# Kernel optimization log

Hardware: AMD Instinct MI355X
Metric: run time of the kernel (lower is better)

Reference implementation:

```python
import jax, jax.numpy as jnp
import numpy as np

B, N, CS, CZ, H, CH, G, P = 2, 384, 384, 128, 8, 16, 2, 8
CZ4 = CZ // 4
INF = 1e5
UMAX = 3.0     # self.u_max
LMAX = 2.0     # self.log_scale_max
SQRT_CH = CH ** 0.5


def quat_to_rot(q):
    q = q / jnp.linalg.norm(q, axis=-1, keepdims=True)
    w, x, y, z = q[..., 0], q[..., 1], q[..., 2], q[..., 3]
    R = jnp.stack([
        1 - 2 * (y * y + z * z), 2 * (x * y - w * z), 2 * (x * z + w * y),
        2 * (x * y + w * z), 1 - 2 * (x * x + z * z), 2 * (y * z - w * x),
        2 * (x * z - w * y), 2 * (y * z + w * x), 1 - 2 * (x * x + y * y)], axis=-1)
    return R.reshape(q.shape[:-1] + (3, 3))


def robust_nll(delta, sigma):
    # inline robust 3x3 Cholesky solve: dist_sq = d^T S^-1 d, log_det = ln|S|
    eps = 1e-8
    s00 = sigma[..., 0, 0]; s01 = sigma[..., 0, 1]; s02 = sigma[..., 0, 2]
    s11 = sigma[..., 1, 1]; s12 = sigma[..., 1, 2]; s22 = sigma[..., 2, 2]
    d0 = delta[..., 0]; d1 = delta[..., 1]; d2 = delta[..., 2]
    l00_sq = jnp.maximum(s00, eps); inv_l00 = jax.lax.rsqrt(l00_sq)
    l10 = s01 * inv_l00; l20 = s02 * inv_l00
    l11_sq = jnp.maximum(s11 - l10 * l10, eps); inv_l11 = jax.lax.rsqrt(l11_sq)
    l21 = (s12 - l20 * l10) * inv_l11
    l22_sq = jnp.maximum(s22 - l20 * l20 - l21 * l21, eps); inv_l22 = jax.lax.rsqrt(l22_sq)
    log_det = jnp.log(l00_sq) + jnp.log(l11_sq) + jnp.log(l22_sq)
    y0 = d0 * inv_l00
    y1 = (d1 - l10 * y0) * inv_l11
    y2 = (d2 - l20 * y0 - l21 * y1) * inv_l22
    return y0 * y0 + y1 * y1 + y2 * y2, log_det


def iga_forward(s, z, mask, rot, trans, local_mean, scaling_log,
                Wq, Wk, Wv, Wb, bb, Wdz, bdz, Wqg, bqg, Wkg, bkg,
                Wvp, bvp, geo_scale, geo_bias, Wout, bout):
    # scalar q/k/v: [B,H,N,CH]
    q = (s @ Wq).reshape(B, N, H, CH).transpose(0, 2, 1, 3)
    k = (s @ Wk).reshape(B, N, H, CH).transpose(0, 2, 1, 3)
    v = (s @ Wv).reshape(B, N, H, CH).transpose(0, 2, 1, 3)
    logits = jnp.einsum('bhid,bhjd->bhij', q, k) / SQRT_CH
    # pair bias: [B,H,N,N]
    logits = logits + (z @ Wb + bb).transpose(0, 3, 1, 2)

    def parse(feat):  # -> u [B,N,H,G,3], s_log_delta [B,N,H,G,3]
        raw = feat.reshape(B, N, H, G, 6)
        return jnp.tanh(raw[..., :3]) * UMAX, jnp.tanh(raw[..., 3:]) * LMAX

    def to_global(u, sld):
        anchor = local_mean[:, :, None, None, :]
        base = scaling_log[:, :, None, None, :]
        sig_loc = jnp.maximum(jnp.exp(base + sld), 1e-6)
        pos = anchor + u * sig_loc
        mu = jnp.einsum('bnij,bnhgj->bnhgi', rot, pos) + trans[:, :, None, None, :]
        var = jnp.exp(2.0 * (base + sld))
        Sig = jnp.einsum('bnij,bnhgj,bnkj->bnhgik', rot, var, rot)  # R diag(var) R^T
        return mu.transpose(0, 2, 1, 3, 4), Sig.transpose(0, 2, 1, 3, 4, 5)

    qu, qs = parse(s @ Wqg + bqg)
    ku, ks = parse(s @ Wkg + bkg)
    q_mu, q_sig = to_global(qu, qs)   # [B,H,N,G,3], [B,H,N,G,3,3]
    k_mu, k_sig = to_global(ku, ks)
    delta = q_mu[:, :, :, None] - k_mu[:, :, None, :]      # [B,H,N,N,G,3]
    ssum = q_sig[:, :, :, None] + k_sig[:, :, None, :]     # [B,H,N,N,G,3,3]
    dist_sq, log_det = robust_nll(delta, ssum)
    geo = (-0.5 * dist_sq - 0.5 * log_det).sum(-1)          # [B,H,N,N]

    mask2d = mask[:, None, :, None] * mask[:, None, None, :]  # [B,1,N,N]
    a = jax.nn.softplus(geo_scale)[None, :, None, None]
    G_geo = a * (geo * mask2d) + geo_bias[None, :, None, None]
    logits = logits + G_geo + (1.0 - mask2d) * (-INF)
    w = jax.nn.softmax(logits, axis=-1)                      # [B,H,N,N]

    # scalar output
    o = jnp.einsum('bhij,bhjd->bihd', w, v).reshape(B, N, H * CH)
    # point output (IPA-style): to global, attend, back to local frame
    vpts = (s @ Wvp + bvp).reshape(B, N, H, P, 3)
    vpg = jnp.einsum('bnij,bnhpj->bnhpi', rot, vpts) + trans[:, :, None, None, :]
    vpg = vpg.transpose(0, 2, 1, 3, 4)                       # [B,H,N,P,3]
    opt = jnp.einsum('bhij,bhjpc->bhipc', w, vpg)            # [B,H,N,P,3]
    opt_local = jnp.einsum('bnji,bhnpj->bnhpi', rot, opt - trans[:, None, :, None, :])
    onorm = jnp.sqrt((opt_local ** 2).sum(-1) + 1e-8)        # [B,N,H,P]
    # pair output
    pz = z @ Wdz + bdz                                       # [B,N,N,CZ4]
    opair = jnp.einsum('bhij,bijc->bihc', w, pz)             # [B,N,H,CZ4]

    cat = jnp.concatenate([o, opt_local.reshape(B, N, H * P * 3),
                           onorm.reshape(B, N, H * P),
                           opair.reshape(B, N, H * CZ4)], axis=-1)  # [B,N,640]
    return cat @ Wout + bout


def setup_inputs() -> dict:
    ks = jax.random.split(jax.random.key(0), 24)
    rnd = lambda i, shape, sc=1.0: jax.random.normal(ks[i], shape, dtype=jnp.float32) * sc
    w = 0.02
    return dict(
        s=rnd(0, (B, N, CS)), z=rnd(1, (B, N, N, CZ)),
        mask=jnp.ones((B, N), jnp.float32),
        rot=quat_to_rot(rnd(2, (B, N, 4))),
        trans=rnd(3, (B, N, 3), 1.0),
        local_mean=rnd(4, (B, N, 3), 0.5),
        scaling_log=rnd(5, (B, N, 3), 0.1),
        Wq=rnd(6, (CS, H * CH), w), Wk=rnd(7, (CS, H * CH), w), Wv=rnd(8, (CS, H * CH), w),
        Wb=rnd(9, (CZ, H), w), bb=rnd(10, (H,), w),
        Wdz=rnd(11, (CZ, CZ4), w), bdz=rnd(12, (CZ4,), w),
        Wqg=rnd(13, (CS, H * G * 6), w), bqg=rnd(14, (H * G * 6,), w),
        Wkg=rnd(15, (CS, H * G * 6), w), bkg=rnd(16, (H * G * 6,), w),
        Wvp=rnd(17, (CS, H * P * 3), w), bvp=rnd(18, (H * P * 3,), w),
        geo_scale=jnp.ones((H,), jnp.float32), geo_bias=jnp.zeros((H,), jnp.float32),
        Wout=rnd(19, (H * (CH + P * 4 + CZ4), CS), w), bout=jnp.zeros((CS,), jnp.float32))


def reference(s, z, mask, rot, trans, local_mean, scaling_log, Wq, Wk, Wv, Wb, bb,
              Wdz, bdz, Wqg, bqg, Wkg, bkg, Wvp, bvp, geo_scale, geo_bias, Wout, bout):
    return iga_forward(s, z, mask, rot, trans, local_mean, scaling_log, Wq, Wk, Wv,
                       Wb, bb, Wdz, bdz, Wqg, bqg, Wkg, bkg, Wvp, bvp,
                       geo_scale, geo_bias, Wout, bout)
```

## Files before the change

kernel.cpp:

```cpp
#include <hip/hip_runtime.h>
#include <hip/hip_fp16.h>

#define NB   2
#define NN   384
#define NCS  384
#define NCZ  128
#define NH   8
#define NCH  16
#define NG   2
#define NP   8
#define NCZ4 32
#define BN   (NB*NN)
#define LINW 768
#define PZROW ((size_t)BN*NN)

typedef _Float16 f16x8 __attribute__((ext_vector_type(8)));
typedef float    f32x4 __attribute__((ext_vector_type(4)));

__global__ void k_wprep(const float* __restrict__ Wb, const float* __restrict__ Wdz,
                        _Float16* __restrict__ wf) {
    int t = threadIdx.x;
    for (int e = t; e < 12*64*8; e += 256) {
        int r = e & 7, lane = (e >> 3) & 63, nk = e >> 9;
        int n = nk >> 2, kk = nk & 3;
        int c = kk*32 + (lane >> 4)*8 + r;
        int col = n*16 + (lane & 15);
        float w;
        if      (col < 8)  w = Wb[c*NH + col];
        else if (col < 40) w = Wdz[c*NCZ4 + (col-8)];
        else               w = 0.f;
        wf[e] = (_Float16)w;
    }
}

__global__ void __launch_bounds__(256, 2)
k_zproj(const float* __restrict__ z, const _Float16* __restrict__ wf,
        const float* __restrict__ bb, const float* __restrict__ bdz,
        float* __restrict__ zbg, __half* __restrict__ pzg2) {
    __shared__ __align__(16) _Float16 zh[64*128];
    __shared__ float  zbT[8][64];
    __shared__ __half pzt[64][34];
    __shared__ float  bias_s[48];

    int t = threadIdx.x;
    int lane = t & 63, w = t >> 6;
    int bi = blockIdx.x / 6, ch = blockIdx.x % 6;
    const float* zbase = z + ((size_t)bi*NN + ch*64)*NCZ;

    const float* src = zbase + (size_t)(t >> 5)*NCZ + (t & 31)*4;
    float4 pre[8];
    #pragma unroll
    for (int p = 0; p < 8; ++p) pre[p] = *(const float4*)(src + (size_t)(p*8)*NCZ);

    f16x8 bfr[12];
    #pragma unroll
    for (int nk = 0; nk < 12; ++nk)
        bfr[nk] = ((const f16x8*)wf)[nk*64 + lane];
    if (t < 48) bias_s[t] = (t < 8) ? bb[t] : ((t < 40) ? bdz[t-8] : 0.f);

    int srow0 = t >> 5;
    int scb   = (t & 31) * 8;
    int sswz  = (srow0 & 7) << 4;
    #pragma unroll
    for (int p = 0; p < 8; ++p) {
        union { _Float16 h[4]; unsigned long long u; } pk;
        pk.h[0] = (_Float16)pre[p].x; pk.h[1] = (_Float16)pre[p].y;
        pk.h[2] = (_Float16)pre[p].z; pk.h[3] = (_Float16)pre[p].w;
        *(unsigned long long*)((char*)zh + (p*8 + srow0)*256 + (scb ^ sswz)) = pk.u;
    }
    __syncthreads();

    int arow  = w*16 + (lane & 15);
    int abase = arow*256 + ((lane >> 4) << 4);
    int akey  = (lane & 7) << 4;
    int ccol  = lane & 15;
    int cjl   = w*16 + (lane >> 4)*4;
    f16x8 af0 = *(const f16x8*)((const char*)zh + ((abase +   0) ^ akey));
    f16x8 af1 = *(const f16x8*)((const char*)zh + ((abase +  64) ^ akey));
    f16x8 af2 = *(const f16x8*)((const char*)zh + ((abase + 128) ^ akey));
    f16x8 af3 = *(const f16x8*)((const char*)zh + ((abase + 192) ^ akey));
    f32x4 ac0 = {0.f,0.f,0.f,0.f}, ac1 = ac0, ac2 = ac0;
    ac0 = __builtin_amdgcn_mfma_f32_16x16x32_f16(af0, bfr[0], ac0, 0,0,0);
    ac1 = __builtin_amdgcn_mfma_f32_16x16x32_f16(af0, bfr[4], ac1, 0,0,0);
    ac2 = __builtin_amdgcn_mfma_f32_16x16x32_f16(af0, bfr[8], ac2, 0,0,0);
    ac0 = __builtin_amdgcn_mfma_f32_16x16x32_f16(af1, bfr[1], ac0, 0,0,0);
    ac1 = __builtin_amdgcn_mfma_f32_16x16x32_f16(af1, bfr[5], ac1, 0,0,0);
    ac2 = __builtin_amdgcn_mfma_f32_16x16x32_f16(af1, bfr[9], ac2, 0,0,0);
    ac0 = __builtin_amdgcn_mfma_f32_16x16x32_f16(af2, bfr[2], ac0, 0,0,0);
    ac1 = __builtin_amdgcn_mfma_f32_16x16x32_f16(af2, bfr[6], ac1, 0,0,0);
    ac2 = __builtin_amdgcn_mfma_f32_16x16x32_f16(af2, bfr[10], ac2, 0,0,0);
    ac0 = __builtin_amdgcn_mfma_f32_16x16x32_f16(af3, bfr[3], ac0, 0,0,0);
    ac1 = __builtin_amdgcn_mfma_f32_16x16x32_f16(af3, bfr[7], ac1, 0,0,0);
    ac2 = __builtin_amdgcn_mfma_f32_16x16x32_f16(af3, bfr[11], ac2, 0,0,0);
    #pragma unroll
    for (int r = 0; r < 4; ++r) {
        int j = cjl + r;
        float v0 = ac0[r] + bias_s[ccol];
        if (ccol < 8) zbT[ccol][j] = v0;
        else          pzt[j][ccol-8] = __float2half(v0);
        pzt[j][ccol+8] = __float2half(ac1[r] + bias_s[16+ccol]);
        if (ccol < 8)
            pzt[j][ccol+24] = __float2half(ac2[r] + bias_s[32+ccol]);
    }
    __syncthreads();

    {
        int e = t*2, h = e >> 6, j = e & 63;
        float2 v; v.x = zbT[h][j]; v.y = zbT[h][j+1];
        *(float2*)(zbg + ((size_t)bi*NH + h)*NN + ch*64 + j) = v;
    }
    {
        int cp = t >> 4, l = t & 15, j0 = l*4;
        union { __half2 h2[4]; float4 f4; } u;
        #pragma unroll
        for (int r = 0; r < 4; ++r) {
            int j = j0 + r;
            u.h2[r] = __halves2half2(pzt[j][2*cp], pzt[j][2*cp+1]);
        }
        __half2* dst = (__half2*)pzg2 + (size_t)cp*PZROW + (size_t)bi*NN + ch*64 + j0;
        *(float4*)dst = u.f4;
    }
}

__global__ void k_rowlin(const float* __restrict__ s,
                         const float* __restrict__ Wq, const float* __restrict__ Wk,
                         const float* __restrict__ Wv,
                         const float* __restrict__ Wqg, const float* __restrict__ bqg,
                         const float* __restrict__ Wkg, const float* __restrict__ bkg,
                         const float* __restrict__ Wvp, const float* __restrict__ bvp,
                         float* __restrict__ lin,
                         float* __restrict__ kT, float* __restrict__ vT) {
    __shared__ float sl[4][NCS];
    int t  = threadIdx.x;
    int r0 = blockIdx.x * 4;
    for (int idx = t; idx < 4*NCS; idx += 256)
        sl[idx / NCS][idx % NCS] = s[(size_t)(r0 + idx/NCS)*NCS + (idx % NCS)];
    __syncthreads();
    int col = blockIdx.y * 256 + t;
    const float* W; int sw; float bias = 0.f;
    if      (col < 128) { W = Wq  + col;        sw = 128; }
    else if (col < 256) { W = Wk  + (col-128);  sw = 128; }
    else if (col < 384) { W = Wv  + (col-256);  sw = 128; }
    else if (col < 480) { W = Wqg + (col-384);  sw = 96;  bias = bqg[col-384]; }
    else if (col < 576) { W = Wkg + (col-480);  sw = 96;  bias = bkg[col-480]; }
    else                { W = Wvp + (col-576);  sw = 192; bias = bvp[col-576]; }
    float a0=0.f, a1=0.f, a2=0.f, a3=0.f;
    for (int c = 0; c < NCS; ++c) {
        float w = W[(size_t)c*sw];
        a0 = fmaf(sl[0][c], w, a0);
        a1 = fmaf(sl[1][c], w, a1);
        a2 = fmaf(sl[2][c], w, a2);
        a3 = fmaf(sl[3][c], w, a3);
    }
    lin[(size_t)(r0+0)*LINW + col] = a0 + bias;
    lin[(size_t)(r0+1)*LINW + col] = a1 + bias;
    lin[(size_t)(r0+2)*LINW + col] = a2 + bias;
    lin[(size_t)(r0+3)*LINW + col] = a3 + bias;
    if (col >= 128 && col < 384) {
        f32x4 v4; v4[0]=a0; v4[1]=a1; v4[2]=a2; v4[3]=a3;
        float* dst = (col < 256) ? (kT + (size_t)(col-128)*BN + r0)
                                 : (vT + (size_t)(col-256)*BN + r0);
        *(f32x4*)dst = v4;
    }
}

__global__ void k_geom(const float* __restrict__ lin, const float* __restrict__ rot,
                       const float* __restrict__ trans, const float* __restrict__ lm,
                       const float* __restrict__ sc,
                       float* __restrict__ qmu, float* __restrict__ qsig,
                       float* __restrict__ kmuT, float* __restrict__ ksigT,
                       float* __restrict__ vpgT) {
    int bn = blockIdx.x, t = threadIdx.x;
    __shared__ float R[9], T[3], A[3], Bs[3];
    if (t < 9) R[t] = rot[bn*9 + t];
    if (t < 3) { T[t] = trans[bn*3+t]; A[t] = lm[bn*3+t]; Bs[t] = sc[bn*3+t]; }
    __syncthreads();
    {
        int h = t >> 3, p = t & 7;
        const float* vr = lin + (size_t)bn*LINW + 576 + h*24 + p*3;
        float x = vr[0], y = vr[1], z = vr[2];
        int e = h*24 + p*3;
        vpgT[(size_t)(e+0)*BN + bn] = R[0]*x + R[1]*y + R[2]*z + T[0];
        vpgT[(size_t)(e+1)*BN + bn] = R[3]*x + R[4]*y + R[5]*z + T[1];
        vpgT[(size_t)(e+2)*BN + bn] = R[6]*x + R[7]*y + R[8]*z + T[2];
    }
    if (t < 32) {
        int side = t >> 4, item = t & 15;
        const float* raw = lin + (size_t)bn*LINW + (side ? 480 : 384) + item*6;
        float u0 = tanhf(raw[0])*3.f, u1 = tanhf(raw[1])*3.f, u2 = tanhf(raw[2])*3.f;
        float e0 = Bs[0] + tanhf(raw[3])*2.f;
        float e1 = Bs[1] + tanhf(raw[4])*2.f;
        float e2 = Bs[2] + tanhf(raw[5])*2.f;
        float sl0 = fmaxf(expf(e0), 1e-6f);
        float sl1 = fmaxf(expf(e1), 1e-6f);
        float sl2 = fmaxf(expf(e2), 1e-6f);
        float p0 = A[0] + u0*sl0, p1 = A[1] + u1*sl1, p2 = A[2] + u2*sl2;
        float mu0 = R[0]*p0 + R[1]*p1 + R[2]*p2 + T[0];
        float mu1 = R[3]*p0 + R[4]*p1 + R[5]*p2 + T[1];
        float mu2 = R[6]*p0 + R[7]*p1 + R[8]*p2 + T[2];
        float v0 = expf(2.f*e0), v1 = expf(2.f*e1), v2 = expf(2.f*e2);
        float s00 = R[0]*R[0]*v0 + R[1]*R[1]*v1 + R[2]*R[2]*v2;
        float s01 = R[0]*R[3]*v0 + R[1]*R[4]*v1 + R[2]*R[5]*v2;
        float s02 = R[0]*R[6]*v0 + R[1]*R[7]*v1 + R[2]*R[8]*v2;
        float s11 = R[3]*R[3]*v0 + R[4]*R[4]*v1 + R[5]*R[5]*v2;
        float s12 = R[3]*R[6]*v0 + R[4]*R[7]*v1 + R[5]*R[8]*v2;
        float s22 = R[6]*R[6]*v0 + R[7]*R[7]*v1 + R[8]*R[8]*v2;
        if (side) {
            kmuT[(size_t)(item*3+0)*BN + bn] = mu0;
            kmuT[(size_t)(item*3+1)*BN + bn] = mu1;
            kmuT[(size_t)(item*3+2)*BN + bn] = mu2;
            ksigT[(size_t)(item*6+0)*BN + bn] = s00;
            ksigT[(size_t)(item*6+1)*BN + bn] = s01;
            ksigT[(size_t)(item*6+2)*BN + bn] = s02;
            ksigT[(size_t)(item*6+3)*BN + bn] = s11;
            ksigT[(size_t)(item*6+4)*BN + bn] = s12;
            ksigT[(size_t)(item*6+5)*BN + bn] = s22;
        } else {
            float* mud = qmu + (size_t)bn*48 + item*3;
            mud[0]=mu0; mud[1]=mu1; mud[2]=mu2;
            float* sgd = qsig + (size_t)bn*96 + item*6;
            sgd[0]=s00; sgd[1]=s01; sgd[2]=s02; sgd[3]=s11; sgd[4]=s12; sgd[5]=s22;
        }
    }
}

__global__ void __launch_bounds__(256, 2)
k_attn2(const float* __restrict__ mask,
        const float* __restrict__ rot, const float* __restrict__ trans,
        const float* __restrict__ lin,
        const float* __restrict__ qmu, const float* __restrict__ qsig,
        const float* __restrict__ kmuT, const float* __restrict__ ksigT,
        const float* __restrict__ kT, const float* __restrict__ vT,
        const float* __restrict__ vpgT,
        const float* __restrict__ zbg, const __half* __restrict__ pzg2,
        const float* __restrict__ gsc, const float* __restrict__ gbi,
        float* __restrict__ cat) {
    __shared__ float  logits[NH][NN];
    __shared__ float  qrow[128];
    __shared__ float  qmu_s[48], qsig_s[96];
    __shared__ float  Rm[9], Tv[3];
    __shared__ float  aH[NH], bH[NH];
    __shared__ float  maskI;

    int t  = threadIdx.x;
    int b  = blockIdx.x / NN, i = blockIdx.x % NN;
    int bi = b*NN + i;
    const size_t boff = (size_t)b*NN;

    if (t < 128) qrow[t] = lin[(size_t)bi*LINW + t];
    if (t < 48)  qmu_s[t] = qmu[(size_t)bi*48 + t];
    if (t >= 64 && t < 160) qsig_s[t-64] = qsig[(size_t)bi*96 + (t-64)];
    if (t >= 160 && t < 169) Rm[t-160] = rot[bi*9 + (t-160)];
    if (t >= 169 && t < 172) Tv[t-169] = trans[bi*3 + (t-169)];
    if (t >= 176 && t < 184) {
        int h = t-176;
        float x = gsc[h];
        aH[h] = (x > 20.f) ? x : log1pf(expf(x));
        bH[h] = gbi[h];
    }
    if (t == 255) maskI = mask[bi];
    __syncthreads();

    int h = t >> 5, lnn = t & 31;
    {
        float qv[16];
        #pragma unroll
        for (int d = 0; d < 16; ++d) qv[d] = qrow[h*16 + d];
        float qm[6], qs[12];
        #pragma unroll
        for (int e = 0; e < 6; ++e)  qm[e] = qmu_s[h*6 + e];
        #pragma unroll
        for (int e = 0; e < 12; ++e) qs[e] = qsig_s[h*12 + e];
        float ascale = aH[h], hbias = bH[h], mI = maskI;
        #pragma unroll 1
        for (int jj = 0; jj < 3; ++jj) {
            int j4 = jj*128 + lnn*4;
            const float* kp = kT + (size_t)(h*16)*BN + boff + j4;
            f32x4 qk = {0.f,0.f,0.f,0.f};
            #pragma unroll
            for (int d = 0; d < 16; ++d) {
                f32x4 kv = *(const f32x4*)(kp + (size_t)d*BN);
                #pragma unroll
                for (int r = 0; r < 4; ++r) qk[r] = fmaf(qv[d], kv[r], qk[r]);
            }
            f32x4 geo = {0.f,0.f,0.f,0.f};
            #pragma unroll
            for (int g = 0; g < NG; ++g) {
                const float* kmb = kmuT + (size_t)((h*2+g)*3)*BN + boff + j4;
                f32x4 km0 = *(const f32x4*)(kmb);
                f32x4 km1 = *(const f32x4*)(kmb + BN);
                f32x4 km2 = *(const f32x4*)(kmb + 2*BN);
                const float* ksb = ksigT + (size_t)((h*2+g)*6)*BN + boff + j4;
                f32x4 ks0 = *(const f32x4*)(ksb);
                f32x4 ks1 = *(const f32x4*)(ksb + BN);
                f32x4 ks2 = *(const f32x4*)(ksb + 2*BN);
                f32x4 ks3 = *(const f32x4*)(ksb + 3*BN);
                f32x4 ks4 = *(const f32x4*)(ksb + 4*BN);
                f32x4 ks5 = *(const f32x4*)(ksb + 5*BN);
                #pragma unroll
                for (int r = 0; r < 4; ++r) {
                    float d0 = qm[g*3+0] - km0[r];
                    float d1 = qm[g*3+1] - km1[r];
                    float d2 = qm[g*3+2] - km2[r];
                    float s00 = qs[g*6+0] + ks0[r];
                    float s01 = qs[g*6+1] + ks1[r];
                    float s02 = qs[g*6+2] + ks2[r];
                    float s11 = qs[g*6+3] + ks3[r];
                    float s12 = qs[g*6+4] + ks4[r];
                    float s22 = qs[g*6+5] + ks5[r];
                    float l00 = fmaxf(s00, 1e-8f);
                    float i00 = rsqrtf(l00);
                    float l10 = s01*i00, l20 = s02*i00;
                    float l11 = fmaxf(s11 - l10*l10, 1e-8f);
                    float i11 = rsqrtf(l11);
                    float l21 = (s12 - l20*l10)*i11;
                    float l22 = fmaxf(s22 - l20*l20 - l21*l21, 1e-8f);
                    float i22 = rsqrtf(l22);
                    float ld = __logf(l00) + __logf(l11) + __logf(l22);
                    float y0 = d0*i00;
                    float y1 = (d1 - l10*y0)*i11;
                    float y2 = (d2 - l20*y0 - l21*y1)*i22;
                    geo[r] += -0.5f*(y0*y0 + y1*y1 + y2*y2 + ld);
                }
            }
            f32x4 zb4 = *(const f32x4*)(zbg + ((size_t)bi*NH + h)*NN + j4);
            f32x4 mv  = *(const f32x4*)(mask + boff + j4);
            f32x4 lg;
            #pragma unroll
            for (int r = 0; r < 4; ++r) {
                float m2 = mI * mv[r];
                lg[r] = qk[r]*0.25f + zb4[r] + ascale*(geo[r]*m2) + hbias
                        + (1.f - m2)*(-100000.f);
            }
            *(f32x4*)&logits[h][j4] = lg;
        }
    }
    __syncthreads();

    float mx = -3.4e38f;
    #pragma unroll
    for (int jj = 0; jj < 12; ++jj) mx = fmaxf(mx, logits[h][lnn + jj*32]);
    #pragma unroll
    for (int m = 16; m >= 1; m >>= 1) mx = fmaxf(mx, __shfl_xor(mx, m, 64));
    float se = 0.f;
    #pragma unroll
    for (int jj = 0; jj < 12; ++jj) {
        int j = lnn + jj*32;
        float e = __expf(logits[h][j] - mx);
        logits[h][j] = e;
        se += e;
    }
    #pragma unroll
    for (int m = 16; m >= 1; m >>= 1) se += __shfl_xor(se, m, 64);
    float inv = 1.f / se;
    float* cp = cat + (size_t)bi*640;

    {
        float o[16];
        #pragma unroll
        for (int d = 0; d < 16; ++d) o[d] = 0.f;
        const float* vbase = vT + (size_t)(h*16)*BN + boff + lnn;
        #pragma unroll 1
        for (int jj = 0; jj < 12; ++jj) {
            float wgt = logits[h][lnn + jj*32] * inv;
            const float* vb = vbase + jj*32;
            #pragma unroll
            for (int d = 0; d < 16; ++d) o[d] = fmaf(wgt, vb[(size_t)d*BN], o[d]);
        }
        #pragma unroll
        for (int m = 16; m >= 1; m >>= 1) {
            #pragma unroll
            for (int d = 0; d < 16; ++d) o[d] += __shfl_xor(o[d], m, 64);
        }
        if (lnn == 0) {
            #pragma unroll
            for (int d = 0; d < 16; ++d) cp[h*16 + d] = o[d];
        }
    }

    {
        float op[24];
        #pragma unroll
        for (int e = 0; e < 24; ++e) op[e] = 0.f;
        const float* gbase = vpgT + (size_t)(h*24)*BN + boff + lnn;
        #pragma unroll 1
        for (int jj = 0; jj < 12; ++jj) {
            float wgt = logits[h][lnn + jj*32] * inv;
            const float* gb = gbase + jj*32;
            #pragma unroll
            for (int e = 0; e < 24; ++e) op[e] = fmaf(wgt, gb[(size_t)e*BN], op[e]);
        }
        #pragma unroll
        for (int m = 16; m >= 1; m >>= 1) {
            #pragma unroll
            for (int e = 0; e < 24; ++e) op[e] += __shfl_xor(op[e], m, 64);
        }
        if (lnn == 0) {
            #pragma unroll
            for (int p = 0; p < 8; ++p) {
                float x  = op[p*3+0] - Tv[0];
                float y  = op[p*3+1] - Tv[1];
                float zz = op[p*3+2] - Tv[2];
                float l0 = Rm[0]*x + Rm[3]*y + Rm[6]*zz;
                float l1 = Rm[1]*x + Rm[4]*y + Rm[7]*zz;
                float l2 = Rm[2]*x + Rm[5]*y + Rm[8]*zz;
                cp[128 + h*24 + p*3 + 0] = l0;
                cp[128 + h*24 + p*3 + 1] = l1;
                cp[128 + h*24 + p*3 + 2] = l2;
                cp[320 + h*8 + p] = sqrtf(l0*l0 + l1*l1 + l2*l2 + 1e-8f);
            }
        }
    }

    {
        float opa[32];
        #pragma unroll
        for (int c = 0; c < 32; ++c) opa[c] = 0.f;
        const __half2* pzb = (const __half2*)pzg2 + (size_t)bi*NN + lnn;
        #pragma unroll 1
        for (int jj = 0; jj < 12; ++jj) {
            float wgt = logits[h][lnn + jj*32] * inv;
            const __half2* pj = pzb + jj*32;
            #pragma unroll
            for (int c2 = 0; c2 < 16; ++c2) {
                float2 pf = __half22float2(pj[c2*PZROW]);
                opa[2*c2]   = fmaf(wgt, pf.x, opa[2*c2]);
                opa[2*c2+1] = fmaf(wgt, pf.y, opa[2*c2+1]);
            }
        }
        #pragma unroll
        for (int m = 16; m >= 1; m >>= 1) {
            #pragma unroll
            for (int c = 0; c < 32; ++c) opa[c] += __shfl_xor(opa[c], m, 64);
        }
        if (lnn == 0) {
            #pragma unroll
            for (int c = 0; c < 32; ++c) cp[384 + h*32 + c] = opa[c];
        }
    }
}

__global__ void k_out(const float* __restrict__ cat, const float* __restrict__ Wout,
                      const float* __restrict__ bout, float* __restrict__ out) {
    __shared__ float cl[4][640];
    int t  = threadIdx.x;
    int r0 = blockIdx.x * 4;
    for (int idx = t; idx < 4*640; idx += 384)
        cl[idx/640][idx%640] = cat[(size_t)(r0 + idx/640)*640 + (idx%640)];
    __syncthreads();
    int col = t;
    float a0=0.f, a1=0.f, a2=0.f, a3=0.f;
    for (int c = 0; c < 640; ++c) {
        float w = Wout[(size_t)c*NCS + col];
        a0 = fmaf(cl[0][c], w, a0);
        a1 = fmaf(cl[1][c], w, a1);
        a2 = fmaf(cl[2][c], w, a2);
        a3 = fmaf(cl[3][c], w, a3);
    }
    float bv = bout[col];
    out[(size_t)(r0+0)*NCS + col] = a0 + bv;
    out[(size_t)(r0+1)*NCS + col] = a1 + bv;
    out[(size_t)(r0+2)*NCS + col] = a2 + bv;
    out[(size_t)(r0+3)*NCS + col] = a3 + bv;
}

extern "C" void kernel_launch(void* const* d_in, const int* in_sizes, int n_in,
                              void* d_out, int out_size, void* d_ws, size_t ws_size,
                              hipStream_t stream) {
    const float* s    = (const float*)d_in[0];
    const float* z    = (const float*)d_in[1];
    const float* mask = (const float*)d_in[2];
    const float* rot  = (const float*)d_in[3];
    const float* trans= (const float*)d_in[4];
    const float* lm   = (const float*)d_in[5];
    const float* sc   = (const float*)d_in[6];
    const float* Wq   = (const float*)d_in[7];
    const float* Wk   = (const float*)d_in[8];
    const float* Wv   = (const float*)d_in[9];
    const float* Wb   = (const float*)d_in[10];
    const float* bb   = (const float*)d_in[11];
    const float* Wdz  = (const float*)d_in[12];
    const float* bdz  = (const float*)d_in[13];
    const float* Wqg  = (const float*)d_in[14];
    const float* bqg  = (const float*)d_in[15];
    const float* Wkg  = (const float*)d_in[16];
    const float* bkg  = (const float*)d_in[17];
    const float* Wvp  = (const float*)d_in[18];
    const float* bvp  = (const float*)d_in[19];
    const float* gsc  = (const float*)d_in[20];
    const float* gbi  = (const float*)d_in[21];
    const float* Wout = (const float*)d_in[22];
    const float* bout = (const float*)d_in[23];
    float* out = (float*)d_out;

    float* ws    = (float*)d_ws;
    float* lin   = ws;
    float* qmu   = lin   + 589824;
    float* qsig  = qmu   + 36864;
    float* kmuT  = qsig  + 73728;
    float* ksigT = kmuT  + 36864;
    float* vpgT  = ksigT + 73728;
    float* kT    = vpgT  + 147456;
    float* vT    = kT    + 98304;
    float* cat   = vT    + 98304;
    float* zbg   = cat   + 491520;
    _Float16* wf = (_Float16*)(zbg + 2359296);
    __half* pzg2 = (__half*)((float*)wf + 3072);

    k_wprep<<<1, 256, 0, stream>>>(Wb, Wdz, wf);
    k_rowlin<<<dim3(192, 3), 256, 0, stream>>>(s, Wq, Wk, Wv, Wqg, bqg, Wkg, bkg,
                                               Wvp, bvp, lin, kT, vT);
    k_geom<<<BN, 64, 0, stream>>>(lin, rot, trans, lm, sc, qmu, qsig, kmuT, ksigT, vpgT);
    k_zproj<<<BN*6, 256, 0, stream>>>(z, wf, bb, bdz, zbg, pzg2);
    k_attn2<<<BN, 256, 0, stream>>>(mask, rot, trans, lin, qmu, qsig, kmuT, ksigT,
                                    kT, vT, vpgT, zbg, pzg2, gsc, gbi, cat);
    k_out<<<192, 384, 0, stream>>>(cat, Wout, bout, out);
}
```

Baseline: 175.5 us.

## Merge weight prep, z projection and row linear into one launch; vectorize attention reductions

Drops the separate weight-prep kernel: each z-projection block now builds its fp16 MFMA B fragments directly from Wb/Wdz in global memory. The z-projection and row-linear kernels are merged into a single heterogeneous grid, so the two independent jobs run together and two launches are saved. The row-linear part now computes 8 rows per block instead of 4, reusing each weight load more. In the attention kernel, the value, point and pair aggregation loops each read 4 contiguous keys per lane with vector loads. The costs are redundant weight gathers in every z block, a changed lane-to-key mapping for the reductions, and register and shared-memory pressure set by the larger branch.

```diff
diff --git a/kernel.cpp b/kernel.cpp
--- a/kernel.cpp
+++ b/kernel.cpp
@@ -13,154 +13,156 @@
 #define BN   (NB*NN)
 #define LINW 768
 #define PZROW ((size_t)BN*NN)
+#define NZB  (BN*6)
+#define NRB  288
 
 typedef _Float16 f16x8 __attribute__((ext_vector_type(8)));
 typedef float    f32x4 __attribute__((ext_vector_type(4)));
 
-__global__ void k_wprep(const float* __restrict__ Wb, const float* __restrict__ Wdz,
-                        _Float16* __restrict__ wf) {
+__global__ void __launch_bounds__(256, 2)
+k_zrow(const float* __restrict__ z,
+       const float* __restrict__ Wb, const float* __restrict__ Wdz,
+       const float* __restrict__ bb, const float* __restrict__ bdz,
+       const float* __restrict__ s,
+       const float* __restrict__ Wq, const float* __restrict__ Wk,
+       const float* __restrict__ Wv,
+       const float* __restrict__ Wqg, const float* __restrict__ bqg,
+       const float* __restrict__ Wkg, const float* __restrict__ bkg,
+       const float* __restrict__ Wvp, const float* __restrict__ bvp,
+       float* __restrict__ zbg, __half* __restrict__ pzg2,
+       float* __restrict__ lin, float* __restrict__ kT, float* __restrict__ vT) {
+    __shared__ __align__(16) char smem[23040];
     int t = threadIdx.x;
-    for (int e = t; e < 12*64*8; e += 256) {
-        int r = e & 7, lane = (e >> 3) & 63, nk = e >> 9;
-        int n = nk >> 2, kk = nk & 3;
-        int c = kk*32 + (lane >> 4)*8 + r;
-        int col = n*16 + (lane & 15);
-        float w;
-        if      (col < 8)  w = Wb[c*NH + col];
-        else if (col < 40) w = Wdz[c*NCZ4 + (col-8)];
-        else               w = 0.f;
-        wf[e] = (_Float16)w;
-    }
-}
-
-__global__ void __launch_bounds__(256, 2)
-k_zproj(const float* __restrict__ z, const _Float16* __restrict__ wf,
-        const float* __restrict__ bb, const float* __restrict__ bdz,
-        float* __restrict__ zbg, __half* __restrict__ pzg2) {
-    __shared__ __align__(16) _Float16 zh[64*128];
-    __shared__ float  zbT[8][64];
-    __shared__ __half pzt[64][34];
-    __shared__ float  bias_s[48];
-
-    int t = threadIdx.x;
-    int lane = t & 63, w = t >> 6;
-    int bi = blockIdx.x / 6, ch = blockIdx.x % 6;
-    const float* zbase = z + ((size_t)bi*NN + ch*64)*NCZ;
-
-    const float* src = zbase + (size_t)(t >> 5)*NCZ + (t & 31)*4;
-    float4 pre[8];
-    #pragma unroll
-    for (int p = 0; p < 8; ++p) pre[p] = *(const float4*)(src + (size_t)(p*8)*NCZ);
-
-    f16x8 bfr[12];
-    #pragma unroll
-    for (int nk = 0; nk < 12; ++nk)
-        bfr[nk] = ((const f16x8*)wf)[nk*64 + lane];
-    if (t < 48) bias_s[t] = (t < 8) ? bb[t] : ((t < 40) ? bdz[t-8] : 0.f);
-
-    int srow0 = t >> 5;
-    int scb   = (t & 31) * 8;
-    int sswz  = (srow0 & 7) << 4;
-    #pragma unroll
-    for (int p = 0; p < 8; ++p) {
-        union { _Float16 h[4]; unsigned long long u; } pk;
-        pk.h[0] = (_Float16)pre[p].x; pk.h[1] = (_Float16)pre[p].y;
-        pk.h[2] = (_Float16)pre[p].z; pk.h[3] = (_Float16)pre[p].w;
-        *(unsigned long long*)((char*)zh + (p*8 + srow0)*256 + (scb ^ sswz)) = pk.u;
-    }
-    __syncthreads();
-
-    int arow  = w*16 + (lane & 15);
-    int abase = arow*256 + ((lane >> 4) << 4);
-    int akey  = (lane & 7) << 4;
-    int ccol  = lane & 15;
-    int cjl   = w*16 + (lane >> 4)*4;
-    f16x8 af0 = *(const f16x8*)((const char*)zh + ((abase +   0) ^ akey));
-    f16x8 af1 = *(const f16x8*)((const char*)zh + ((abase +  64) ^ akey));
-    f16x8 af2 = *(const f16x8*)((const char*)zh + ((abase + 128) ^ akey));
-    f16x8 af3 = *(const f16x8*)((const char*)zh + ((abase + 192) ^ akey));
-    f32x4 ac0 = {0.f,0.f,0.f,0.f}, ac1 = ac0, ac2 = ac0;
-    ac0 = __builtin_amdgcn_mfma_f32_16x16x32_f16(af0, bfr[0], ac0, 0,0,0);
-    ac1 = __builtin_amdgcn_mfma_f32_16x16x32_f16(af0, bfr[4], ac1, 0,0,0);
-    ac2 = __builtin_amdgcn_mfma_f32_16x16x32_f16(af0, bfr[8], ac2, 0,0,0);
-    ac0 = __builtin_amdgcn_mfma_f32_16x16x32_f16(af1, bfr[1], ac0, 0,0,0);
-    ac1 = __builtin_amdgcn_mfma_f32_16x16x32_f16(af1, bfr[5], ac1, 0,0,0);
-    ac2 = __builtin_amdgcn_mfma_f32_16x16x32_f16(af1, bfr[9], ac2, 0,0,0);
-    ac0 = __builtin_amdgcn_mfma_f32_16x16x32_f16(af2, bfr[2], ac0, 0,0,0);
-    ac1 = __builtin_amdgcn_mfma_f32_16x16x32_f16(af2, bfr[6], ac1, 0,0,0);
-    ac2 = __builtin_amdgcn_mfma_f32_16x16x32_f16(af2, bfr[10], ac2, 0,0,0);
-    ac0 = __builtin_amdgcn_mfma_f32_16x16x32_f16(af3, bfr[3], ac0, 0,0,0);
-    ac1 = __builtin_amdgcn_mfma_f32_16x16x32_f16(af3, bfr[7], ac1, 0,0,0);
-    ac2 = __builtin_amdgcn_mfma_f32_16x16x32_f16(af3, bfr[11], ac2, 0,0,0);
-    #pragma unroll
-    for (int r = 0; r < 4; ++r) {
-        int j = cjl + r;
-        float v0 = ac0[r] + bias_s[ccol];
-        if (ccol < 8) zbT[ccol][j] = v0;
-        else          pzt[j][ccol-8] = __float2half(v0);
-        pzt[j][ccol+8] = __float2half(ac1[r] + bias_s[16+ccol]);
-        if (ccol < 8)
-            pzt[j][ccol+24] = __float2half(ac2[r] + bias_s[32+ccol]);
-    }
-    __syncthreads();
-
-    {
-        int e = t*2, h = e >> 6, j = e & 63;
-        float2 v; v.x = zbT[h][j]; v.y = zbT[h][j+1];
-        *(float2*)(zbg + ((size_t)bi*NH + h)*NN + ch*64 + j) = v;
-    }
-    {
-        int cp = t >> 4, l = t & 15, j0 = l*4;
-        union { __half2 h2[4]; float4 f4; } u;
+
+    if (blockIdx.x < NZB) {
+        _Float16* zh = (_Float16*)smem;
+        float (*zbT)[64] = (float(*)[64])(smem + 16384);
+        __half (*pzt)[34] = (__half(*)[34])(smem + 18432);
+        float* bias_s = (float*)(smem + 22784);
+
+        int lane = t & 63, w = t >> 6;
+        int bi = blockIdx.x / 6, ch = blockIdx.x % 6;
+        const float* zbase = z + ((size_t)bi*NN + ch*64)*NCZ;
+
+        const float* src = zbase + (size_t)(t >> 5)*NCZ + (t & 31)*4;
+        float4 pre[8];
+        #pragma unroll
+        for (int p = 0; p < 8; ++p) pre[p] = *(const float4*)(src + (size_t)(p*8)*NCZ);
+
+        f16x8 bfr[12];
+        #pragma unroll
+        for (int nk = 0; nk < 12; ++nk) {
+            int n = nk >> 2, kk = nk & 3;
+            #pragma unroll
+            for (int r = 0; r < 8; ++r) {
+                int c = kk*32 + (lane >> 4)*8 + r;
+                int col = n*16 + (lane & 15);
+                float wv;
+                if      (col < 8)  wv = Wb[c*NH + col];
+                else if (col < 40) wv = Wdz[c*NCZ4 + (col-8)];
+                else               wv = 0.f;
+                bfr[nk][r] = (_Float16)wv;
+            }
+        }
+        if (t < 48) bias_s[t] = (t < 8) ? bb[t] : ((t < 40) ? bdz[t-8] : 0.f);
+
+        int srow0 = t >> 5;
+        int scb   = (t & 31) * 8;
+        int sswz  = (srow0 & 7) << 4;
+        #pragma unroll
+        for (int p = 0; p < 8; ++p) {
+            union { _Float16 h[4]; unsigned long long u; } pk;
+            pk.h[0] = (_Float16)pre[p].x; pk.h[1] = (_Float16)pre[p].y;
+            pk.h[2] = (_Float16)pre[p].z; pk.h[3] = (_Float16)pre[p].w;
+            *(unsigned long long*)((char*)zh + (p*8 + srow0)*256 + (scb ^ sswz)) = pk.u;
+        }
+        __syncthreads();
+
+        int arow  = w*16 + (lane & 15);
+        int abase = arow*256 + ((lane >> 4) << 4);
+        int akey  = (lane & 7) << 4;
+        int ccol  = lane & 15;
+        int cjl   = w*16 + (lane >> 4)*4;
+        f16x8 af0 = *(const f16x8*)((const char*)zh + ((abase +   0) ^ akey));
+        f16x8 af1 = *(const f16x8*)((const char*)zh + ((abase +  64) ^ akey));
+        f16x8 af2 = *(const f16x8*)((const char*)zh + ((abase + 128) ^ akey));
+        f16x8 af3 = *(const f16x8*)((const char*)zh + ((abase + 192) ^ akey));
+        f32x4 ac0 = {0.f,0.f,0.f,0.f}, ac1 = ac0, ac2 = ac0;
+        ac0 = __builtin_amdgcn_mfma_f32_16x16x32_f16(af0, bfr[0], ac0, 0,0,0);
+        ac1 = __builtin_amdgcn_mfma_f32_16x16x32_f16(af0, bfr[4], ac1, 0,0,0);
+        ac2 = __builtin_amdgcn_mfma_f32_16x16x32_f16(af0, bfr[8], ac2, 0,0,0);
+        ac0 = __builtin_amdgcn_mfma_f32_16x16x32_f16(af1, bfr[1], ac0, 0,0,0);
+        ac1 = __builtin_amdgcn_mfma_f32_16x16x32_f16(af1, bfr[5], ac1, 0,0,0);
+        ac2 = __builtin_amdgcn_mfma_f32_16x16x32_f16(af1, bfr[9], ac2, 0,0,0);
+        ac0 = __builtin_amdgcn_mfma_f32_16x16x32_f16(af2, bfr[2], ac0, 0,0,0);
+        ac1 = __builtin_amdgcn_mfma_f32_16x16x32_f16(af2, bfr[6], ac1, 0,0,0);
+        ac2 = __builtin_amdgcn_mfma_f32_16x16x32_f16(af2, bfr[10], ac2, 0,0,0);
+        ac0 = __builtin_amdgcn_mfma_f32_16x16x32_f16(af3, bfr[3], ac0, 0,0,0);
+        ac1 = __builtin_amdgcn_mfma_f32_16x16x32_f16(af3, bfr[7], ac1, 0,0,0);
+        ac2 = __builtin_amdgcn_mfma_f32_16x16x32_f16(af3, bfr[11], ac2, 0,0,0);
         #pragma unroll
         for (int r = 0; r < 4; ++r) {
-            int j = j0 + r;
-            u.h2[r] = __halves2half2(pzt[j][2*cp], pzt[j][2*cp+1]);
-        }
-        __half2* dst = (__half2*)pzg2 + (size_t)cp*PZROW + (size_t)bi*NN + ch*64 + j0;
-        *(float4*)dst = u.f4;
-    }
-}
-
-__global__ void k_rowlin(const float* __restrict__ s,
-                         const float* __restrict__ Wq, const float* __restrict__ Wk,
-                         const float* __restrict__ Wv,
-                         const float* __restrict__ Wqg, const float* __restrict__ bqg,
-                         const float* __restrict__ Wkg, const float* __restrict__ bkg,
-                         const float* __restrict__ Wvp, const float* __restrict__ bvp,
-                         float* __restrict__ lin,
-                         float* __restrict__ kT, float* __restrict__ vT) {
-    __shared__ float sl[4][NCS];
-    int t  = threadIdx.x;
-    int r0 = blockIdx.x * 4;
-    for (int idx = t; idx < 4*NCS; idx += 256)
-        sl[idx / NCS][idx % NCS] = s[(size_t)(r0 + idx/NCS)*NCS + (idx % NCS)];
-    __syncthreads();
-    int col = blockIdx.y * 256 + t;
-    const float* W; int sw; float bias = 0.f;
-    if      (col < 128) { W = Wq  + col;        sw = 128; }
-    else if (col < 256) { W = Wk  + (col-128);  sw = 128; }
-    else if (col < 384) { W = Wv  + (col-256);  sw = 128; }
-    else if (col < 480) { W = Wqg + (col-384);  sw = 96;  bias = bqg[col-384]; }
-    else if (col < 576) { W = Wkg + (col-480);  sw = 96;  bias = bkg[col-480]; }
-    else                { W = Wvp + (col-576);  sw = 192; bias = bvp[col-576]; }
-    float a0=0.f, a1=0.f, a2=0.f, a3=0.f;
-    for (int c = 0; c < NCS; ++c) {
-        float w = W[(size_t)c*sw];
-        a0 = fmaf(sl[0][c], w, a0);
-        a1 = fmaf(sl[1][c], w, a1);
-        a2 = fmaf(sl[2][c], w, a2);
-        a3 = fmaf(sl[3][c], w, a3);
-    }
-    lin[(size_t)(r0+0)*LINW + col] = a0 + bias;
-    lin[(size_t)(r0+1)*LINW + col] = a1 + bias;
-    lin[(size_t)(r0+2)*LINW + col] = a2 + bias;
-    lin[(size_t)(r0+3)*LINW + col] = a3 + bias;
-    if (col >= 128 && col < 384) {
-        f32x4 v4; v4[0]=a0; v4[1]=a1; v4[2]=a2; v4[3]=a3;
-        float* dst = (col < 256) ? (kT + (size_t)(col-128)*BN + r0)
-                                 : (vT + (size_t)(col-256)*BN + r0);
-        *(f32x4*)dst = v4;
+            int j = cjl + r;
+            float v0 = ac0[r] + bias_s[ccol];
+            if (ccol < 8) zbT[ccol][j] = v0;
+            else          pzt[j][ccol-8] = __float2half(v0);
+            pzt[j][ccol+8] = __float2half(ac1[r] + bias_s[16+ccol]);
+            if (ccol < 8)
+                pzt[j][ccol+24] = __float2half(ac2[r] + bias_s[32+ccol]);
+        }
+        __syncthreads();
+
+        {
+            int e = t*2, h = e >> 6, j = e & 63;
+            float2 v; v.x = zbT[h][j]; v.y = zbT[h][j+1];
+            *(float2*)(zbg + ((size_t)bi*NH + h)*NN + ch*64 + j) = v;
+        }
+        {
+            int cp = t >> 4, l = t & 15, j0 = l*4;
+            union { __half2 h2[4]; float4 f4; } u;
+            #pragma unroll
+            for (int r = 0; r < 4; ++r) {
+                int j = j0 + r;
+                u.h2[r] = __halves2half2(pzt[j][2*cp], pzt[j][2*cp+1]);
+            }
+            __half2* dst = (__half2*)pzg2 + (size_t)cp*PZROW + (size_t)bi*NN + ch*64 + j0;
+            *(float4*)dst = u.f4;
+        }
+    } else {
+        float (*sl)[NCS] = (float(*)[NCS])smem;
+        int rb = blockIdx.x - NZB;
+        int r0 = (rb / 3) * 8;
+        int col = (rb % 3) * 256 + t;
+        for (int idx = t; idx < 8*NCS; idx += 256)
+            sl[idx / NCS][idx % NCS] = s[(size_t)(r0 + idx/NCS)*NCS + (idx % NCS)];
+        __syncthreads();
+        const float* W; int sw; float bias = 0.f;
+        if      (col < 128) { W = Wq  + col;        sw = 128; }
+        else if (col < 256) { W = Wk  + (col-128);  sw = 128; }
+        else if (col < 384) { W = Wv  + (col-256);  sw = 128; }
+        else if (col < 480) { W = Wqg + (col-384);  sw = 96;  bias = bqg[col-384]; }
+        else if (col < 576) { W = Wkg + (col-480);  sw = 96;  bias = bkg[col-480]; }
+        else                { W = Wvp + (col-576);  sw = 192; bias = bvp[col-576]; }
+        float a[8];
+        #pragma unroll
+        for (int r = 0; r < 8; ++r) a[r] = 0.f;
+        for (int c = 0; c < NCS; ++c) {
+            float wv = W[(size_t)c*sw];
+            #pragma unroll
+            for (int r = 0; r < 8; ++r) a[r] = fmaf(sl[r][c], wv, a[r]);
+        }
+        #pragma unroll
+        for (int r = 0; r < 8; ++r)
+            lin[(size_t)(r0+r)*LINW + col] = a[r] + bias;
+        if (col >= 128 && col < 384) {
+            f32x4 v0, v1;
+            #pragma unroll
+            for (int r = 0; r < 4; ++r) { v0[r] = a[r]; v1[r] = a[4+r]; }
+            float* dst = (col < 256) ? (kT + (size_t)(col-128)*BN + r0)
+                                     : (vT + (size_t)(col-256)*BN + r0);
+            *(f32x4*)dst = v0;
+            *(f32x4*)(dst+4) = v1;
+        }
     }
 }
 
@@ -359,13 +361,21 @@
         float o[16];
         #pragma unroll
         for (int d = 0; d < 16; ++d) o[d] = 0.f;
-        const float* vbase = vT + (size_t)(h*16)*BN + boff + lnn;
+        const float* vbase = vT + (size_t)(h*16)*BN + boff;
         #pragma unroll 1
-        for (int jj = 0; jj < 12; ++jj) {
-            float wgt = logits[h][lnn + jj*32] * inv;
-            const float* vb = vbase + jj*32;
-            #pragma unroll
-            for (int d = 0; d < 16; ++d) o[d] = fmaf(wgt, vb[(size_t)d*BN], o[d]);
+        for (int jj = 0; jj < 3; ++jj) {
+            int j4 = jj*128 + lnn*4;
+            f32x4 lg4 = *(const f32x4*)&logits[h][j4];
+            f32x4 w4;
+            #pragma unroll
+            for (int r = 0; r < 4; ++r) w4[r] = lg4[r] * inv;
+            const float* vb = vbase + j4;
+            #pragma unroll
+            for (int d = 0; d < 16; ++d) {
+                f32x4 kv = *(const f32x4*)(vb + (size_t)d*BN);
+                #pragma unroll
+                for (int r = 0; r < 4; ++r) o[d] = fmaf(w4[r], kv[r], o[d]);
+            }
         }
         #pragma unroll
         for (int m = 16; m >= 1; m >>= 1) {
@@ -382,13 +392,21 @@
         float op[24];
         #pragma unroll
         for (int e = 0; e < 24; ++e) op[e] = 0.f;
-        const float* gbase = vpgT + (size_t)(h*24)*BN + boff + lnn;
+        const float* gbase = vpgT + (size_t)(h*24)*BN + boff;
         #pragma unroll 1
-        for (int jj = 0; jj < 12; ++jj) {
-            float wgt = logits[h][lnn + jj*32] * inv;
-            const float* gb = gbase + jj*32;
-            #pragma unroll
-            for (int e = 0; e < 24; ++e) op[e] = fmaf(wgt, gb[(size_t)e*BN], op[e]);
+        for (int jj = 0; jj < 3; ++jj) {
+            int j4 = jj*128 + lnn*4;
+            f32x4 lg4 = *(const f32x4*)&logits[h][j4];
+            f32x4 w4;
+            #pragma unroll
+            for (int r = 0; r < 4; ++r) w4[r] = lg4[r] * inv;
+            const float* gb = gbase + j4;
+            #pragma unroll
+            for (int e = 0; e < 24; ++e) {
+                f32x4 gv = *(const f32x4*)(gb + (size_t)e*BN);
+                #pragma unroll
+                for (int r = 0; r < 4; ++r) op[e] = fmaf(w4[r], gv[r], op[e]);
+            }
         }
         #pragma unroll
         for (int m = 16; m >= 1; m >>= 1) {
@@ -416,16 +434,24 @@
         float opa[32];
         #pragma unroll
         for (int c = 0; c < 32; ++c) opa[c] = 0.f;
-        const __half2* pzb = (const __half2*)pzg2 + (size_t)bi*NN + lnn;
+        const __half2* pzb = (const __half2*)pzg2 + (size_t)bi*NN;
         #pragma unroll 1
-        for (int jj = 0; jj < 12; ++jj) {
-            float wgt = logits[h][lnn + jj*32] * inv;
-            const __half2* pj = pzb + jj*32;
+        for (int jj = 0; jj < 3; ++jj) {
+            int j4 = jj*128 + lnn*4;
+            f32x4 lg4 = *(const f32x4*)&logits[h][j4];
+            f32x4 w4;
+            #pragma unroll
+            for (int r = 0; r < 4; ++r) w4[r] = lg4[r] * inv;
             #pragma unroll
             for (int c2 = 0; c2 < 16; ++c2) {
-                float2 pf = __half22float2(pj[c2*PZROW]);
-                opa[2*c2]   = fmaf(wgt, pf.x, opa[2*c2]);
-                opa[2*c2+1] = fmaf(wgt, pf.y, opa[2*c2+1]);
+                union { float4 f4; __half2 h2[4]; } u;
+                u.f4 = *(const float4*)(pzb + (size_t)c2*PZROW + j4);
+                #pragma unroll
+                for (int r = 0; r < 4; ++r) {
+                    float2 pf = __half22float2(u.h2[r]);
+                    opa[2*c2]   = fmaf(w4[r], pf.x, opa[2*c2]);
+                    opa[2*c2+1] = fmaf(w4[r], pf.y, opa[2*c2+1]);
+                }
             }
         }
         #pragma unroll
@@ -504,14 +530,12 @@
     float* vT    = kT    + 98304;
     float* cat   = vT    + 98304;
     float* zbg   = cat   + 491520;
-    _Float16* wf = (_Float16*)(zbg + 2359296);
-    __half* pzg2 = (__half*)((float*)wf + 3072);
-
-    k_wprep<<<1, 256, 0, stream>>>(Wb, Wdz, wf);
-    k_rowlin<<<dim3(192, 3), 256, 0, stream>>>(s, Wq, Wk, Wv, Wqg, bqg, Wkg, bkg,
-                                               Wvp, bvp, lin, kT, vT);
+    __half* pzg2 = (__half*)(zbg + 2359296);
+
+    k_zrow<<<NZB + NRB, 256, 0, stream>>>(z, Wb, Wdz, bb, bdz, s,
+                                          Wq, Wk, Wv, Wqg, bqg, Wkg, bkg, Wvp, bvp,
+                                          zbg, pzg2, lin, kT, vT);
     k_geom<<<BN, 64, 0, stream>>>(lin, rot, trans, lm, sc, qmu, qsig, kmuT, ksigT, vpgT);
-    k_zproj<<<BN*6, 256, 0, stream>>>(z, wf, bb, bdz, zbg, pzg2);
     k_attn2<<<BN, 256, 0, stream>>>(mask, rot, trans, lin, qmu, qsig, kmuT, ksigT,
                                     kT, vT, vpgT, zbg, pzg2, gsc, gbi, cat);
     k_out<<<192, 384, 0, stream>>>(cat, Wout, bout, out);
```

Measured after the change: 180.1 us. 2.6% more time.
